# Optimization experiments

Hardware: AMD Instinct MI355X
Metric: run time of the kernel (lower is better)

The kernel has to match this reference:

```python
import jax, jax.numpy as jnp
import numpy as np

THRESHOLD = 0.5        # correspondence distance threshold (init kwarg)
MAX_ITERS = 50         # fixed iteration count (open3d's max_iteration)
EPS = 1e-6


def setup_inputs() -> dict:
    key = jax.random.key(0)
    k1, k2 = jax.random.split(key)
    B, N, M = 8, 2048, 2048
    source = jax.random.normal(k1, (B, N, 3), dtype=jnp.float32)
    target = jax.random.normal(k2, (B, M, 3), dtype=jnp.float32)
    return {"source": source, "target": target}


def _icp(source, target):
    """Batched point-to-point ICP. source: (B,N,3), target: (B,M,3) -> (B,4,4)."""
    B, N, _ = source.shape
    dt = source.dtype
    t_sq = jnp.sum(target * target, axis=-1)  # (B,M), constant across iterations

    def step(T, _):
        R, tr = T[:, :3, :3], T[:, :3, 3]
        src = jnp.einsum('bij,bnj->bni', R, source) + tr[:, None, :]  # (B,N,3)
        # brute-force nearest neighbor: squared distances (B,N,M)
        d2 = (jnp.sum(src * src, axis=-1)[:, :, None]
              - 2.0 * jnp.einsum('bnd,bmd->bnm', src, target)
              + t_sq[:, None, :])
        idx = jnp.argmin(d2, axis=-1)                                   # (B,N)
        mind2 = jnp.take_along_axis(d2, idx[..., None], axis=-1)[..., 0]
        nn = jnp.take_along_axis(target, idx[..., None], axis=1)        # (B,N,3)
        # inlier mask: correspondences within threshold
        w = (mind2 < THRESHOLD * THRESHOLD).astype(dt)                  # (B,N)
        wsum = jnp.maximum(jnp.sum(w, axis=-1, keepdims=True), EPS)     # (B,1)
        cs = jnp.sum(w[..., None] * src, axis=1) / wsum                 # (B,3)
        ct = jnp.sum(w[..., None] * nn, axis=1) / wsum                  # (B,3)
        Sc = src - cs[:, None, :]
        Tc = nn - ct[:, None, :]
        # cross-covariance H = sum_n w_n (s_n - cs)(t_n - ct)^T  -> (B,3,3)
        H = jnp.einsum('bn,bni,bnj->bij', w, Sc, Tc)
        U, _, Vh = jnp.linalg.svd(H, full_matrices=False)
        V = jnp.swapaxes(Vh, -1, -2)
        # reflection fix (Kabsch): R = V diag(1,1,sign(det(V U^T))) U^T
        d = jnp.sign(jnp.linalg.det(jnp.einsum('bij,bkj->bik', V, U)))
        scale = jnp.stack([jnp.ones_like(d), jnp.ones_like(d), d], axis=-1)
        Rd = jnp.einsum('bij,bj,bkj->bik', V, scale, U)                 # (B,3,3)
        td = ct - jnp.einsum('bij,bj->bi', Rd, cs)                      # (B,3)
        top = jnp.concatenate([Rd, td[:, :, None]], axis=-1)            # (B,3,4)
        bot = jnp.broadcast_to(jnp.array([0., 0., 0., 1.], dtype=dt), (B, 1, 4))
        delta = jnp.concatenate([top, bot], axis=1)                     # (B,4,4)
        return jnp.einsum('bij,bjk->bik', delta, T), None

    T0 = jnp.broadcast_to(jnp.eye(4, dtype=dt), (B, 4, 4))
    Tfin, _ = jax.lax.scan(step, T0, None, length=MAX_ITERS)
    return Tfin


def reference(source, target):
    return _icp(source, target)
```

## Files before the change

### kernel.cpp

```cpp
#include <hip/hip_runtime.h>
#include <stdint.h>

#define BATCH 8
#define NPTS 2048
#define MPTS 2048
#define ITERS 50
#define THR2 0.25f
#define CHUNKS 32
#define SRC_PER_BLOCK 64
#define PTS 8
#define NTHREADS 1024
#define NWAVES 16
#define SLICE_LEN 16

__global__ __launch_bounds__(NTHREADS)
void icp_kernel(const float* __restrict__ src,
                const float* __restrict__ tgt,
                float* __restrict__ out,
                float* __restrict__ ws)
{
    const int tid   = threadIdx.x;
    const int blk   = blockIdx.x;
    const int b     = blk >> 5;
    const int chunk = blk & 31;
    const int g     = tid & 7;
    const int s     = tid >> 3;
    const int lane  = tid & 63;
    const int wv    = tid >> 6;

    __shared__ float4 tgt4[MPTS];
    __shared__ float  red[NWAVES][65];
    __shared__ float  srcP[SRC_PER_BLOCK][3];
    __shared__ float4 bcastT4[3];

    const float* tb = tgt + (size_t)b * MPTS * 3;
    for (int m = tid; m < MPTS; m += NTHREADS) {
        float tx = tb[m*3+0], ty = tb[m*3+1], tz = tb[m*3+2];
        tgt4[m] = make_float4(-2.f*tx, -2.f*ty, -2.f*tz, tx*tx + ty*ty + tz*tz);
    }
    const float* sb = src + (size_t)b * NPTS * 3 + (size_t)chunk * SRC_PER_BLOCK * 3;
    if (tid < SRC_PER_BLOCK) {
        srcP[tid][0] = sb[tid*3+0];
        srcP[tid][1] = sb[tid*3+1];
        srcP[tid][2] = sb[tid*3+2];
    }
    float px[PTS], py[PTS], pz[PTS];
#pragma unroll
    for (int r = 0; r < PTS; ++r) {
        int i = g*PTS + r;
        px[r] = sb[i*3+0]; py[r] = sb[i*3+1]; pz[r] = sb[i*3+2];
    }
    __syncthreads();

    float r00=1.f,r01=0.f,r02=0.f, r10=0.f,r11=1.f,r12=0.f, r20=0.f,r21=0.f,r22=1.f;
    float t0=0.f,t1=0.f,t2=0.f;

    unsigned int* bar = (unsigned int*)ws;
    float* slots = ws + 512;

    for (int it = 0; it < ITERS; ++it) {
        float sx[PTS], sy[PTS], sz[PTS];
#pragma unroll
        for (int r = 0; r < PTS; ++r) {
            sx[r] = r00*px[r] + r01*py[r] + r02*pz[r] + t0;
            sy[r] = r10*px[r] + r11*py[r] + r12*pz[r] + t1;
            sz[r] = r20*px[r] + r21*py[r] + r22*pz[r] + t2;
        }
        float best[PTS];
#pragma unroll
        for (int r = 0; r < PTS; ++r) best[r] = __int_as_float(0x7F800000);

        const int base = s * SLICE_LEN;
#pragma unroll 8
        for (int i = 0; i < SLICE_LEN; ++i) {
            int jo = (i + s) & (SLICE_LEN - 1);
            int jj = base + jo;
            float4 q = tgt4[jj];
#pragma unroll
            for (int r = 0; r < PTS; ++r) {
                float d = fmaf(sx[r], q.x, fmaf(sy[r], q.y, fmaf(sz[r], q.z, q.w)));
                unsigned int pd = (__float_as_uint(d) & 0xFFFFF800u) | (unsigned int)jj;
                best[r] = fminf(best[r], __uint_as_float(pd));
            }
        }
#pragma unroll
        for (int r = 0; r < PTS; ++r) {
            float v = best[r];
            v = fminf(v, __shfl_xor(v, 8, 64));
            v = fminf(v, __shfl_xor(v, 16, 64));
            v = fminf(v, __shfl_xor(v, 32, 64));
            best[r] = v;
        }
        if (lane < 8) {
#pragma unroll
            for (int r = 0; r < PTS; ++r) red[wv][lane*PTS + r] = best[r];
        }
        __syncthreads();

        if (tid < 64) {
            float m = red[0][tid];
#pragma unroll
            for (int ww = 1; ww < NWAVES; ++ww) m = fminf(m, red[ww][tid]);
            unsigned int mb = __float_as_uint(m);
            int   bi   = (int)(mb & 0x7FFu);
            float dmin = __uint_as_float(mb & 0xFFFFF800u);

            float ppx = srcP[tid][0], ppy = srcP[tid][1], ppz = srcP[tid][2];
            float qx = r00*ppx + r01*ppy + r02*ppz + t0;
            float qy = r10*ppx + r11*ppy + r12*ppz + t1;
            float qz = r20*ppx + r21*ppy + r22*ppz + t2;
            float s2 = qx*qx + qy*qy + qz*qz;
            float w = (dmin + s2 < THR2) ? 1.f : 0.f;
            float4 nnq = tgt4[bi];
            float nx = -0.5f*nnq.x, ny = -0.5f*nnq.y, nz = -0.5f*nnq.z;

            float v[16];
            v[0]=w;      v[1]=w*qx;    v[2]=w*qy;    v[3]=w*qz;
            v[4]=w*nx;   v[5]=w*ny;    v[6]=w*nz;
            v[7]=w*qx*nx;  v[8]=w*qx*ny;  v[9]=w*qx*nz;
            v[10]=w*qy*nx; v[11]=w*qy*ny; v[12]=w*qy*nz;
            v[13]=w*qz*nx; v[14]=w*qz*ny; v[15]=w*qz*nz;
#pragma unroll
            for (int j = 0; j < 16; ++j) {
                float a = v[j];
#pragma unroll
                for (int off = 1; off < 64; off <<= 1) a += __shfl_xor(a, off, 64);
                v[j] = a;
            }
            if (tid == 0) {
                float* sp = slots + (((size_t)(it & 1) * BATCH + b) * CHUNKS + chunk) * 16;
#pragma unroll
                for (int j = 0; j < 16; ++j)
                    __hip_atomic_store(&sp[j], v[j], __ATOMIC_RELAXED, __HIP_MEMORY_SCOPE_AGENT);
                asm volatile("s_waitcnt vmcnt(0)" ::: "memory");
                __hip_atomic_fetch_add(&bar[b*64], 1u, __ATOMIC_RELAXED, __HIP_MEMORY_SCOPE_AGENT);
                unsigned int target = (unsigned int)(CHUNKS * (it + 1));
                while (__hip_atomic_load(&bar[b*64], __ATOMIC_RELAXED, __HIP_MEMORY_SCOPE_AGENT) < target) {
                    __builtin_amdgcn_s_sleep(1);
                }
                asm volatile("" ::: "memory");
            }
            float S_own = 0.f;
            if (tid < 16) {
                const float* gp = slots + (((size_t)(it & 1) * BATCH + b) * CHUNKS) * 16 + tid;
                float lv[CHUNKS];
#pragma unroll
                for (int c = 0; c < CHUNKS; ++c)
                    lv[c] = __hip_atomic_load(&gp[c*16], __ATOMIC_RELAXED, __HIP_MEMORY_SCOPE_AGENT);
#pragma unroll
                for (int c = 0; c < CHUNKS; ++c) S_own += lv[c];
            }
            float S[16];
#pragma unroll
            for (int j = 0; j < 16; ++j) S[j] = __shfl(S_own, j, 64);

            float wsum = fmaxf(S[0], 1e-6f);
            float inv  = 1.f / wsum;
            float ax=S[1], ay=S[2], az=S[3], bx=S[4], by=S[5], bz=S[6];
            float H00=S[7] -ax*bx*inv, H01=S[8] -ax*by*inv, H02=S[9] -ax*bz*inv;
            float H10=S[10]-ay*bx*inv, H11=S[11]-ay*by*inv, H12=S[12]-ay*bz*inv;
            float H20=S[13]-az*bx*inv, H21=S[14]-az*by*inv, H22=S[15]-az*bz*inv;

            float a00 = H00*H00 + H10*H10 + H20*H20;
            float a01 = H00*H01 + H10*H11 + H20*H21;
            float a02 = H00*H02 + H10*H12 + H20*H22;
            float a11 = H01*H01 + H11*H11 + H21*H21;
            float a12 = H01*H02 + H11*H12 + H21*H22;
            float a22 = H02*H02 + H12*H12 + H22*H22;

            float v00=1.f,v01=0.f,v02=0.f, v10=0.f,v11=1.f,v12=0.f, v20=0.f,v21=0.f,v22=1.f;

            auto rot = [](float &app, float &aqq, float &apq,
                          float &arp, float &arq,
                          float &vp0, float &vq0, float &vp1, float &vq1, float &vp2, float &vq2) {
                float q = apq;
                if (fabsf(q) > 1e-20f) {
                    float tau = (aqq - app) / (2.f * q);
                    float tt  = (tau >= 0.f ? 1.f : -1.f) / (fabsf(tau) + sqrtf(1.f + tau*tau));
                    float c   = 1.f / sqrtf(1.f + tt*tt);
                    float sn  = tt * c;
                    app -= tt * q;
                    aqq += tt * q;
                    apq = 0.f;
                    float x = arp, y = arq;
                    arp = c*x - sn*y;  arq = sn*x + c*y;
                    float u, w2;
                    u = vp0; w2 = vq0; vp0 = c*u - sn*w2; vq0 = sn*u + c*w2;
                    u = vp1; w2 = vq1; vp1 = c*u - sn*w2; vq1 = sn*u + c*w2;
                    u = vp2; w2 = vq2; vp2 = c*u - sn*w2; vq2 = sn*u + c*w2;
                }
            };
#pragma unroll
            for (int sw = 0; sw < 5; ++sw) {
                rot(a00, a11, a01, a02, a12, v00, v01, v10, v11, v20, v21);
                rot(a00, a22, a02, a01, a12, v00, v02, v10, v12, v20, v22);
                rot(a11, a22, a12, a01, a02, v01, v02, v11, v12, v21, v22);
            }
            {
                float tmp;
                if (a00 < a11) { tmp=a00;a00=a11;a11=tmp; tmp=v00;v00=v01;v01=tmp; tmp=v10;v10=v11;v11=tmp; tmp=v20;v20=v21;v21=tmp; }
                if (a00 < a22) { tmp=a00;a00=a22;a22=tmp; tmp=v00;v00=v02;v02=tmp; tmp=v10;v10=v12;v12=tmp; tmp=v20;v20=v22;v22=tmp; }
                if (a11 < a22) { tmp=a11;a11=a22;a22=tmp; tmp=v01;v01=v02;v02=tmp; tmp=v11;v11=v12;v12=tmp; tmp=v21;v21=v22;v22=tmp; }
            }

            float Rd00=1.f,Rd01=0.f,Rd02=0.f, Rd10=0.f,Rd11=1.f,Rd12=0.f, Rd20=0.f,Rd21=0.f,Rd22=1.f;
            {
                float u0x = H00*v00 + H01*v10 + H02*v20;
                float u0y = H10*v00 + H11*v10 + H12*v20;
                float u0z = H20*v00 + H21*v10 + H22*v20;
                float n0 = sqrtf(u0x*u0x + u0y*u0y + u0z*u0z);
                if (n0 > 1e-20f) {
                    float in0 = 1.f/n0; u0x*=in0; u0y*=in0; u0z*=in0;
                    float u1x = H00*v01 + H01*v11 + H02*v21;
                    float u1y = H10*v01 + H11*v11 + H12*v21;
                    float u1z = H20*v01 + H21*v11 + H22*v21;
                    float d01 = u0x*u1x + u0y*u1y + u0z*u1z;
                    u1x -= d01*u0x; u1y -= d01*u0y; u1z -= d01*u0z;
                    float n1 = sqrtf(u1x*u1x + u1y*u1y + u1z*u1z);
                    if (!(n1 > 1e-20f)) {
                        float fx = fabsf(u0x), fy = fabsf(u0y), fz = fabsf(u0z);
                        float ex=0.f, ey=0.f, ez=0.f;
                        if (fx <= fy && fx <= fz) ex = 1.f; else if (fy <= fz) ey = 1.f; else ez = 1.f;
                        u1x = u0y*ez - u0z*ey; u1y = u0z*ex - u0x*ez; u1z = u0x*ey - u0y*ex;
                        n1 = sqrtf(u1x*u1x + u1y*u1y + u1z*u1z);
                    }
                    float in1 = 1.f/n1; u1x*=in1; u1y*=in1; u1z*=in1;
                    float u2x = u0y*u1z - u0z*u1y;
                    float u2y = u0z*u1x - u0x*u1z;
                    float u2z = u0x*u1y - u0y*u1x;
                    float detV = v00*(v11*v22 - v12*v21) - v01*(v10*v22 - v12*v20) + v02*(v10*v21 - v11*v20);
                    float dsg = (detV >= 0.f) ? 1.f : -1.f;
                    Rd00 = v00*u0x + v01*u1x + dsg*v02*u2x;
                    Rd01 = v00*u0y + v01*u1y + dsg*v02*u2y;
                    Rd02 = v00*u0z + v01*u1z + dsg*v02*u2z;
                    Rd10 = v10*u0x + v11*u1x + dsg*v12*u2x;
                    Rd11 = v10*u0y + v11*u1y + dsg*v12*u2y;
                    Rd12 = v10*u0z + v11*u1z + dsg*v12*u2z;
                    Rd20 = v20*u0x + v21*u1x + dsg*v22*u2x;
                    Rd21 = v20*u0y + v21*u1y + dsg*v22*u2y;
                    Rd22 = v20*u0z + v21*u1z + dsg*v22*u2z;
                }
            }
            float csx = ax*inv, csy = ay*inv, csz = az*inv;
            float ctx = bx*inv, cty = by*inv, ctz = bz*inv;
            float tdx = ctx - (Rd00*csx + Rd01*csy + Rd02*csz);
            float tdy = cty - (Rd10*csx + Rd11*csy + Rd12*csz);
            float tdz = ctz - (Rd20*csx + Rd21*csy + Rd22*csz);

            float nr00 = Rd00*r00 + Rd01*r10 + Rd02*r20;
            float nr01 = Rd00*r01 + Rd01*r11 + Rd02*r21;
            float nr02 = Rd00*r02 + Rd01*r12 + Rd02*r22;
            float nr10 = Rd10*r00 + Rd11*r10 + Rd12*r20;
            float nr11 = Rd10*r01 + Rd11*r11 + Rd12*r21;
            float nr12 = Rd10*r02 + Rd11*r12 + Rd12*r22;
            float nr20 = Rd20*r00 + Rd21*r10 + Rd22*r20;
            float nr21 = Rd20*r01 + Rd21*r11 + Rd22*r21;
            float nr22 = Rd20*r02 + Rd21*r12 + Rd22*r22;
            float nt0 = Rd00*t0 + Rd01*t1 + Rd02*t2 + tdx;
            float nt1 = Rd10*t0 + Rd11*t1 + Rd12*t2 + tdy;
            float nt2 = Rd20*t0 + Rd21*t1 + Rd22*t2 + tdz;

            if (tid == 0) {
                bcastT4[0] = make_float4(nr00, nr01, nr02, nt0);
                bcastT4[1] = make_float4(nr10, nr11, nr12, nt1);
                bcastT4[2] = make_float4(nr20, nr21, nr22, nt2);
            }
        }
        __syncthreads();
        {
            float4 tA = bcastT4[0], tB = bcastT4[1], tC = bcastT4[2];
            r00=tA.x; r01=tA.y; r02=tA.z; t0=tA.w;
            r10=tB.x; r11=tB.y; r12=tB.z; t1=tB.w;
            r20=tC.x; r21=tC.y; r22=tC.z; t2=tC.w;
        }
    }

    if (chunk == 0 && tid == 0) {
        float* o = out + (size_t)b * 16;
        o[0]=r00;  o[1]=r01;  o[2]=r02;  o[3]=t0;
        o[4]=r10;  o[5]=r11;  o[6]=r12;  o[7]=t1;
        o[8]=r20;  o[9]=r21;  o[10]=r22; o[11]=t2;
        o[12]=0.f; o[13]=0.f; o[14]=0.f; o[15]=1.f;
    }
}

extern "C" void kernel_launch(void* const* d_in, const int* in_sizes, int n_in,
                              void* d_out, int out_size, void* d_ws, size_t ws_size,
                              hipStream_t stream) {
    const float* src = (const float*)d_in[0];
    const float* tgt = (const float*)d_in[1];
    float* out = (float*)d_out;
    float* ws  = (float*)d_ws;

    hipMemsetAsync(d_ws, 0, 2048, stream);

    void* args[] = { (void*)&src, (void*)&tgt, (void*)&out, (void*)&ws };
    hipLaunchCooperativeKernel((const void*)icp_kernel,
                               dim3(BATCH * CHUNKS), dim3(NTHREADS),
                               args, 0, stream);
}
```

Baseline: 571.3 us.

## Replace counter barrier with iteration-tagged 64-bit partial-sum slots polled by one wave

Each chunk now writes its 16 partial sums as 64-bit words that pack the iteration number in the high half and the float value in the low half. A whole wave polls all 32x16 slots for the batch until every tag matches, then stages the values through shared memory for the final reduction. This removes the atomic counter increment, the spin on a shared counter, and the second pass of global loads that followed the barrier. In exchange, each polling round loads more data and the wave spins on many global addresses.

```diff
diff --git a/kernel.cpp b/kernel.cpp
--- a/kernel.cpp
+++ b/kernel.cpp
@@ -31,6 +31,7 @@
     __shared__ float4 tgt4[MPTS];
     __shared__ float  red[NWAVES][65];
     __shared__ float  srcP[SRC_PER_BLOCK][3];
+    __shared__ float  gsum[CHUNKS][17];
     __shared__ float4 bcastT4[3];
 
     const float* tb = tgt + (size_t)b * MPTS * 3;
@@ -55,8 +56,7 @@
     float r00=1.f,r01=0.f,r02=0.f, r10=0.f,r11=1.f,r12=0.f, r20=0.f,r21=0.f,r22=1.f;
     float t0=0.f,t1=0.f,t2=0.f;
 
-    unsigned int* bar = (unsigned int*)ws;
-    float* slots = ws + 512;
+    unsigned long long* slot64 = (unsigned long long*)ws;
 
     for (int it = 0; it < ITERS; ++it) {
         float sx[PTS], sy[PTS], sz[PTS];
@@ -127,28 +127,43 @@
                 for (int off = 1; off < 64; off <<= 1) a += __shfl_xor(a, off, 64);
                 v[j] = a;
             }
-            if (tid == 0) {
-                float* sp = slots + (((size_t)(it & 1) * BATCH + b) * CHUNKS + chunk) * 16;
-#pragma unroll
-                for (int j = 0; j < 16; ++j)
-                    __hip_atomic_store(&sp[j], v[j], __ATOMIC_RELAXED, __HIP_MEMORY_SCOPE_AGENT);
-                asm volatile("s_waitcnt vmcnt(0)" ::: "memory");
-                __hip_atomic_fetch_add(&bar[b*64], 1u, __ATOMIC_RELAXED, __HIP_MEMORY_SCOPE_AGENT);
-                unsigned int target = (unsigned int)(CHUNKS * (it + 1));
-                while (__hip_atomic_load(&bar[b*64], __ATOMIC_RELAXED, __HIP_MEMORY_SCOPE_AGENT) < target) {
-                    __builtin_amdgcn_s_sleep(1);
+            const unsigned int want = (unsigned int)(it + 1);
+            const size_t base64 = ((size_t)(it & 1) * BATCH + b) * (CHUNKS * 16);
+
+            {
+                float myv = 0.f;
+#pragma unroll
+                for (int j = 0; j < 16; ++j) if ((lane & 15) == j) myv = v[j];
+                if (lane < 16) {
+                    unsigned long long p = ((unsigned long long)want << 32)
+                                         | (unsigned long long)__float_as_uint(myv);
+                    __hip_atomic_store(&slot64[base64 + (size_t)chunk * 16 + lane], p,
+                                       __ATOMIC_RELAXED, __HIP_MEMORY_SCOPE_AGENT);
                 }
+            }
+            {
+                unsigned long long got[8];
+                bool ok;
+                do {
+#pragma unroll
+                    for (int k = 0; k < 8; ++k)
+                        got[k] = __hip_atomic_load(&slot64[base64 + (size_t)k * 64 + lane],
+                                                   __ATOMIC_RELAXED, __HIP_MEMORY_SCOPE_AGENT);
+                    unsigned int vo = 1u;
+#pragma unroll
+                    for (int k = 0; k < 8; ++k)
+                        vo &= (unsigned int)((unsigned int)(got[k] >> 32) == want);
+                    ok = __all(vo != 0u);
+                } while (!ok);
                 asm volatile("" ::: "memory");
+#pragma unroll
+                for (int k = 0; k < 8; ++k)
+                    gsum[k*4 + (lane >> 4)][lane & 15] = __uint_as_float((unsigned int)got[k]);
             }
             float S_own = 0.f;
             if (tid < 16) {
-                const float* gp = slots + (((size_t)(it & 1) * BATCH + b) * CHUNKS) * 16 + tid;
-                float lv[CHUNKS];
-#pragma unroll
-                for (int c = 0; c < CHUNKS; ++c)
-                    lv[c] = __hip_atomic_load(&gp[c*16], __ATOMIC_RELAXED, __HIP_MEMORY_SCOPE_AGENT);
-#pragma unroll
-                for (int c = 0; c < CHUNKS; ++c) S_own += lv[c];
+#pragma unroll
+                for (int c = 0; c < CHUNKS; ++c) S_own += gsum[c][tid];
             }
             float S[16];
 #pragma unroll
@@ -292,7 +307,7 @@
     float* out = (float*)d_out;
     float* ws  = (float*)d_ws;
 
-    hipMemsetAsync(d_ws, 0, 2048, stream);
+    hipMemsetAsync(d_ws, 0, 2 * BATCH * CHUNKS * 16 * sizeof(unsigned long long), stream);
 
     void* args[] = { (void*)&src, (void*)&tgt, (void*)&out, (void*)&ws };
     hipLaunchCooperativeKernel((const void*)icp_kernel,
```

Result: faster. 522.8 us (-8.5%).
